# Optimization experiments

Measured on AMD Instinct MI355X. Metric: run time of the kernel, lower is better.

Reference implementation:

```python
import jax, jax.numpy as jnp
from jax import lax
import numpy as np

N, C, D, KNN = 32768, 1000, 1024, 16
EPS_EUC = 1e-12
EPS_COS = 1e-8
COS_THRESH = 0.85


def setup_inputs() -> dict:
    key = jax.random.key(0)
    k1, k2, k3 = jax.random.split(key, 3)
    feature = jax.random.normal(k1, (N, D), dtype=jnp.float32)
    pred = jax.random.normal(k2, (N, C), dtype=jnp.float32)
    unlabeled_index = jnp.arange(N, dtype=jnp.int64) if jax.config.jax_enable_x64 else jnp.arange(N, dtype=jnp.int32)
    # module state: centroids (from FeaturePool), top-N score buffer (init -1), fake index buffer (init -1)
    centroids = jax.random.normal(k3, (C, D), dtype=jnp.float32)
    pred_top_N = jnp.full((C, KNN), -1.0, dtype=jnp.float32)
    fake_index = jnp.full((C, KNN), -1, dtype=jnp.int32)
    return {"feature": feature, "pred": pred, "unlabeled_index": unlabeled_index,
            "centroids": centroids, "pred_top_N": pred_top_N, "fake_index": fake_index}


def reference(feature, pred, unlabeled_index, centroids, pred_top_N, fake_index):
    xx = jnp.sum(feature * feature, axis=1, keepdims=True)          # [N,1]
    yy = jnp.sum(centroids * centroids, axis=1)[None, :]            # [1,C]
    euc = jnp.sqrt(jnp.clip(xx + yy - 2.0 * (feature @ centroids.T), EPS_EUC, None))
    euc_id = jnp.argmin(euc, axis=1)                                # [N]

    scores = jnp.max(jax.nn.softmax(pred, axis=1), axis=1)          # [N] max softmax prob

    # cosine similarity of every sample to every centroid [N, C]
    f_n = feature / jnp.clip(jnp.linalg.norm(feature, axis=1, keepdims=True), EPS_COS, None)
    c_n = centroids / jnp.clip(jnp.linalg.norm(centroids, axis=1, keepdims=True), EPS_COS, None)
    cos = f_n @ c_n.T
    label_idx = jnp.argmax(cos, axis=1)                             # [N]
    cos_max = jnp.max(cos, axis=1)                                  # [N]

    # label[i] = label_idx if (cos-argmax == euc-argmin and cos_max > 0.85) else -1
    label = jnp.where((label_idx == euc_id) & (cos_max > COS_THRESH),
                      label_idx.astype(jnp.float32), -1.0)

    # sequential bounded top-N scatter update of (pred_top_N, fake_index)
    def step(carry, x):
        ptn, fidx = carry
        li, sc, ui = x
        row = ptn[li]                        # [KNN]
        mi = jnp.argmin(row)
        upd = sc > row[mi]
        ptn = ptn.at[li, mi].set(jnp.where(upd, sc, row[mi]))
        fidx = fidx.at[li, mi].set(jnp.where(upd, ui.astype(fidx.dtype), fidx[li, mi]))
        return (ptn, fidx), None

    (ptn_new, fidx_new), _ = lax.scan(step, (pred_top_N, fake_index),
                                      (label_idx, scores, unlabeled_index))
    return label, ptn_new, fidx_new
```

## Files before the change

kernel.cpp:

```cpp
#include <hip/hip_runtime.h>
#include <hip/hip_bf16.h>
#include <math.h>

#define NS 32768
#define NC 1000
#define CP 1024
#define DD 1024
#define KN 16

typedef __attribute__((ext_vector_type(8))) short bf16x8;
typedef __attribute__((ext_vector_type(4))) float f32x4;
typedef __attribute__((ext_vector_type(4))) float float4v;
typedef __attribute__((ext_vector_type(4))) int int4v;
typedef __attribute__((ext_vector_type(8))) unsigned short u16x8;
typedef __attribute__((ext_vector_type(4))) unsigned short u16x4;

__device__ __forceinline__ unsigned short f2bf(float f) {
  unsigned u = __float_as_uint(f);
  u += 0x7FFFu + ((u >> 16) & 1u);
  return (unsigned short)(u >> 16);
}
__device__ __forceinline__ float bf2f(unsigned short h) {
  return __uint_as_float(((unsigned)h) << 16);
}

#define GLL16(g, l) __builtin_amdgcn_global_load_lds( \
    (const __attribute__((address_space(1))) void*)(g), \
    (__attribute__((address_space(3))) void*)(l), 16, 0, 0)

__global__ __launch_bounds__(256) void k_cast_cent(
    const float* __restrict__ Cm, unsigned short* __restrict__ Cb,
    float* __restrict__ cnorm2, float* __restrict__ invc) {
  int c = blockIdx.x;
  int tid = threadIdx.x;
  float sq = 0.f;
  if (c < NC) {
    float4v v = ((const float4v*)(Cm + (size_t)c * DD))[tid];
    sq = v[0]*v[0] + v[1]*v[1] + v[2]*v[2] + v[3]*v[3];
    u16x4 o = { f2bf(v[0]), f2bf(v[1]), f2bf(v[2]), f2bf(v[3]) };
    *(u16x4*)(Cb + (size_t)c * DD + tid * 4) = o;
  } else {
    u16x4 z = { 0, 0, 0, 0 };
    *(u16x4*)(Cb + (size_t)c * DD + tid * 4) = z;
  }
  for (int off = 32; off; off >>= 1) sq += __shfl_xor(sq, off);
  __shared__ float red[4];
  int lane = tid & 63, wid = tid >> 6;
  if (!lane) red[wid] = sq;
  __syncthreads();
  if (!tid) {
    float s = red[0] + red[1] + red[2] + red[3];
    cnorm2[c] = s;
    float n = sqrtf(s); if (n < 1e-8f) n = 1e-8f;
    invc[c] = (c < NC) ? 1.0f / n : 0.0f;
  }
}

__global__ __launch_bounds__(256) void k_cast_feat(
    const float* __restrict__ A, unsigned short* __restrict__ Ab) {
  int t = blockIdx.x * 256 + threadIdx.x;
  const float4v* src = (const float4v*)A + (size_t)t * 2;
  float4v a = src[0], b = src[1];
  u16x8 o = { f2bf(a[0]), f2bf(a[1]), f2bf(a[2]), f2bf(a[3]),
              f2bf(b[0]), f2bf(b[1]), f2bf(b[2]), f2bf(b[3]) };
  *(u16x8*)(Ab + (size_t)t * 8) = o;
}

#define MF(a_, b_, c_) __builtin_amdgcn_mfma_f32_16x16x32_bf16(a_, b_, c_, 0, 0, 0)
#define RD(base_, i_) (*(const bf16x8*)((base_) + (i_) * 1024 + aoff))
#define SA(s_, b_) do { \
    GLL16(pA0 + (s_) * 32, ldsB + (b_) * 16384 + dA0); \
    GLL16(pA1 + (s_) * 32, ldsB + (b_) * 16384 + dA1); } while (0)
#define SB(s_, b_) do { \
    GLL16(pB0 + (s_) * 32, ldsB + 65536 + (b_) * 16384 + dA0); \
    GLL16(pB1 + (s_) * 32, ldsB + 65536 + (b_) * 16384 + dA1); } while (0)
#define VM4 asm volatile("s_waitcnt vmcnt(4)" ::: "memory")
#define VM0 asm volatile("s_waitcnt vmcnt(0)" ::: "memory")
#define MFMAC(A0_, A1_, A2_, A3_, M0) do { \
    acc[M0+0][0] = MF(A0_, bv0, acc[M0+0][0]); \
    acc[M0+0][1] = MF(A0_, bv1, acc[M0+0][1]); \
    acc[M0+0][2] = MF(A0_, bv2, acc[M0+0][2]); \
    acc[M0+0][3] = MF(A0_, bv3, acc[M0+0][3]); \
    acc[M0+1][0] = MF(A1_, bv0, acc[M0+1][0]); \
    acc[M0+1][1] = MF(A1_, bv1, acc[M0+1][1]); \
    acc[M0+1][2] = MF(A1_, bv2, acc[M0+1][2]); \
    acc[M0+1][3] = MF(A1_, bv3, acc[M0+1][3]); \
    acc[M0+2][0] = MF(A2_, bv0, acc[M0+2][0]); \
    acc[M0+2][1] = MF(A2_, bv1, acc[M0+2][1]); \
    acc[M0+2][2] = MF(A2_, bv2, acc[M0+2][2]); \
    acc[M0+2][3] = MF(A2_, bv3, acc[M0+2][3]); \
    acc[M0+3][0] = MF(A3_, bv0, acc[M0+3][0]); \
    acc[M0+3][1] = MF(A3_, bv1, acc[M0+3][1]); \
    acc[M0+3][2] = MF(A3_, bv2, acc[M0+3][2]); \
    acc[M0+3][3] = MF(A3_, bv3, acc[M0+3][3]); } while (0)
#define KSTEP(s_, STAGE_, GATE_) do { \
    const char* Ab_ = ldsB + ((s_) & 3) * 16384 + wrOff; \
    const char* Bb_ = ldsB + 65536 + ((s_) & 3) * 16384 + wcOff; \
    af0 = RD(Ab_, 0); af1 = RD(Ab_, 1); af2 = RD(Ab_, 2); af3 = RD(Ab_, 3); \
    bv0 = RD(Bb_, 0); bv1 = RD(Bb_, 1); bv2 = RD(Bb_, 2); bv3 = RD(Bb_, 3); \
    af4 = RD(Ab_, 4); af5 = RD(Ab_, 5); af6 = RD(Ab_, 6); af7 = RD(Ab_, 7); \
    STAGE_; \
    __builtin_amdgcn_s_setprio(1); \
    MFMAC(af0, af1, af2, af3, 0); \
    MFMAC(af4, af5, af6, af7, 4); \
    __builtin_amdgcn_s_setprio(0); \
    GATE_; \
    __builtin_amdgcn_s_barrier(); \
  } while (0)

__global__ __launch_bounds__(512, 1) void k_gemm(
    const unsigned short* __restrict__ A,
    const unsigned short* __restrict__ B,
    unsigned short* __restrict__ Dout) {
  __shared__ unsigned short lds[65536];
  char* ldsB = (char*)lds;
  int tid = threadIdx.x, lane = tid & 63, wid = tid >> 6;
  int wr = wid >> 2, wc = wid & 3;
  int bid = (blockIdx.x & 7) * 64 + (blockIdx.x >> 3);
  int cb = bid & 3, rb = bid >> 2;
  int brow = rb * 256, bcol = cb * 256;

  f32x4 acc[8][4];
#pragma unroll
  for (int m = 0; m < 8; ++m)
#pragma unroll
    for (int n = 0; n < 4; ++n) acc[m][n] = (f32x4){0.f, 0.f, 0.f, 0.f};

  int f0 = wid * 64 + lane, f1 = f0 + 512;
  int gl0 = (f0 & 3) ^ ((f0 >> 3) & 3);
  int gl1 = (f1 & 3) ^ ((f1 >> 3) & 3);
  const unsigned short* pA0 = A + (size_t)(brow + (f0 >> 2)) * DD + gl0 * 8;
  const unsigned short* pA1 = A + (size_t)(brow + (f1 >> 2)) * DD + gl1 * 8;
  const unsigned short* pB0 = B + (size_t)(bcol + (f0 >> 2)) * DD + gl0 * 8;
  const unsigned short* pB1 = B + (size_t)(bcol + (f1 >> 2)) * DD + gl1 * 8;
  int dA0 = f0 * 16, dA1 = f1 * 16;

  int aoff = (lane & 15) * 64 + (((lane >> 4) ^ ((lane >> 1) & 3)) * 16);
  int wrOff = wr * 8192;
  int wcOff = wc * 4096;

  bf16x8 af0, af1, af2, af3, af4, af5, af6, af7, bv0, bv1, bv2, bv3;

  SA(0, 0); SB(0, 0);
  SA(1, 1); SB(1, 1);
  VM4;
  __builtin_amdgcn_s_barrier();

  for (int s = 0; s < 30; ++s) {
    int bn = (s + 2) & 3;
    KSTEP(s, { SA(s + 2, bn); SB(s + 2, bn); }, VM4);
  }
  KSTEP(30, (void)0, VM0);
  KSTEP(31, (void)0, (void)0);

  int colb = bcol + wc * 64 + (lane & 15);
  int rowb = brow + wr * 128 + ((lane >> 4) << 2);
#pragma unroll
  for (int m = 0; m < 8; ++m)
#pragma unroll
    for (int n = 0; n < 4; ++n)
#pragma unroll
      for (int j = 0; j < 4; ++j)
        Dout[(size_t)(rowb + m * 16 + j) * CP + colb + n * 16] = f2bf(acc[m][n][j]);
}

__global__ __launch_bounds__(256) void k_score(
    const float* __restrict__ P, float* __restrict__ scores) {
  int i = blockIdx.x, tid = threadIdx.x;
  const float* row = P + (size_t)i * NC;
  bool act = tid < 250;
  float p0 = 0, p1 = 0, p2 = 0, p3 = 0, mx = -1e30f;
  if (act) {
    int b = tid * 4;
    p0 = row[b]; p1 = row[b + 1]; p2 = row[b + 2]; p3 = row[b + 3];
    mx = fmaxf(fmaxf(p0, p1), fmaxf(p2, p3));
  }
  for (int off = 32; off; off >>= 1) mx = fmaxf(mx, __shfl_xor(mx, off));
  __shared__ float wmax[4];
  __shared__ double wsum[4];
  int lane = tid & 63, wid = tid >> 6;
  if (!lane) wmax[wid] = mx;
  __syncthreads();
  float m = fmaxf(fmaxf(wmax[0], wmax[1]), fmaxf(wmax[2], wmax[3]));
  double s = 0.0;
  if (act)
    s = (double)__expf(p0 - m) + (double)__expf(p1 - m) +
        (double)__expf(p2 - m) + (double)__expf(p3 - m);
  for (int off = 32; off; off >>= 1) s += __shfl_xor(s, off);
  if (!lane) wsum[wid] = s;
  __syncthreads();
  if (!tid) scores[i] = (float)(1.0 / (wsum[0] + wsum[1] + wsum[2] + wsum[3]));
}

__global__ __launch_bounds__(256) void k_argmax(
    const unsigned short* __restrict__ Dot, const float* __restrict__ invc,
    const float* __restrict__ cnorm2, const float* __restrict__ feat,
    const float* __restrict__ cent, float* __restrict__ label_out,
    int* __restrict__ lidx) {
  __shared__ float s_inv[CP], s_cn[CP];
  int tid = threadIdx.x;
#pragma unroll
  for (int q = 0; q < 4; ++q) {
    int c = q * 256 + tid;
    s_inv[c] = invc[c]; s_cn[c] = cnorm2[c];
  }
  __syncthreads();
  int lane = tid & 63, wid = tid >> 6;
  int i = blockIdx.x * 4 + wid;
  const unsigned short* drow = Dot + (size_t)i * CP;

  float v[16];
  float dmax = -1e30f; int darg = CP;
  float emin = 1e30f;  int earg = CP;
#pragma unroll
  for (int it = 0; it < 16; ++it) {
    int c = it * 64 + lane;
    float val, ev;
    if (c < NC) {
      float d = bf2f(drow[c]);
      val = d * s_inv[c];
      ev = s_cn[c] - 2.0f * d;
    } else { val = -1e30f; ev = 1e30f; }
    v[it] = val;
    if (val > dmax) { dmax = val; darg = c; }
    if (ev < emin)  { emin = ev;  earg = c; }
  }
  for (int off = 32; off; off >>= 1) {
    float om = __shfl_xor(dmax, off); int oi = __shfl_xor(darg, off);
    if (om > dmax || (om == dmax && oi < darg)) { dmax = om; darg = oi; }
    float oe = __shfl_xor(emin, off); int oj = __shfl_xor(earg, off);
    if (oe < emin || (oe == emin && oj < earg)) { emin = oe; earg = oj; }
  }
  const float MARGIN = 0.15f;
  unsigned long long cmask[16]; int ccnt = 0;
#pragma unroll
  for (int it = 0; it < 16; ++it) {
    int c = it * 64 + lane;
    bool cand = (c < NC) && (v[it] >= dmax - MARGIN);
    cmask[it] = __ballot(cand);
    ccnt += __popcll(cmask[it]);
  }
  int finalArg = darg;
  double cosmax_d = -2.0;
  bool need = (ccnt > 1) || (dmax > 10.0f);
  if (need) {
    float xv[16]; double sx = 0.0;
    const float* xr = feat + (size_t)i * DD;
#pragma unroll
    for (int t = 0; t < 16; ++t) {
      float x = xr[t * 64 + lane]; xv[t] = x; sx += (double)x * (double)x;
    }
    for (int off = 32; off; off >>= 1) sx += __shfl_xor(sx, off);
    double nx = sqrt(sx); if (nx < 1e-8) nx = 1e-8;
    double best = -2.0; int besti = CP;
    for (int it = 0; it < 16; ++it) {
      unsigned long long mk = cmask[it];
      while (mk) {
        int b = __builtin_ctzll(mk); mk &= mk - 1;
        int c = it * 64 + b;
        const float* cr = cent + (size_t)c * DD;
        double s = 0.0, s2 = 0.0;
#pragma unroll
        for (int t = 0; t < 16; ++t) {
          double cv = (double)cr[t * 64 + lane];
          s += (double)xv[t] * cv; s2 += cv * cv;
        }
        for (int off = 32; off; off >>= 1) {
          s += __shfl_xor(s, off); s2 += __shfl_xor(s2, off);
        }
        double nc = sqrt(s2); if (nc < 1e-8) nc = 1e-8;
        double cs = s / (nx * nc);
        if (cs > best) { best = cs; besti = c; }
      }
    }
    finalArg = besti; cosmax_d = best;
  }
  if (!lane) {
    lidx[i] = finalArg;
    float lab = -1.0f;
    if (need && finalArg == earg && cosmax_d > 0.85) lab = (float)finalArg;
    label_out[i] = lab;
  }
}

__global__ __launch_bounds__(64) void k_scan(
    const int* __restrict__ lidx, const float* __restrict__ scores,
    const int* __restrict__ uidx, const float* __restrict__ ptn_in,
    const int* __restrict__ fidx_in, float* __restrict__ out_ptn,
    float* __restrict__ out_fidx) {
  int c = blockIdx.x;
  int lane = threadIdx.x;
  float row[KN]; int idx[KN];
#pragma unroll
  for (int j = 0; j < KN; ++j) {
    row[j] = ptn_in[c * KN + j];
    idx[j] = fidx_in[c * KN + j];
  }
  for (int base = 0; base < NS; base += 256) {
    int l0 = lidx[base + lane];
    int l1 = lidx[base + 64 + lane];
    int l2 = lidx[base + 128 + lane];
    int l3 = lidx[base + 192 + lane];
#pragma unroll
    for (int q = 0; q < 4; ++q) {
      int lab = (q == 0) ? l0 : (q == 1) ? l1 : (q == 2) ? l2 : l3;
      unsigned long long m = __ballot(lab == c);
      while (m) {
        int b = __builtin_ctzll(m); m &= m - 1;
        int i = base + q * 64 + b;
        float s = scores[i];
        int ui = uidx[i];
        int mi = 0; float mn = row[0];
#pragma unroll
        for (int t = 1; t < KN; ++t)
          if (row[t] < mn) { mn = row[t]; mi = t; }
        if (s > mn) {
#pragma unroll
          for (int t = 0; t < KN; ++t)
            if (t == mi) { row[t] = s; idx[t] = ui; }
        }
      }
    }
  }
  if (!lane) {
#pragma unroll
    for (int j = 0; j < KN; ++j) {
      out_ptn[c * KN + j] = row[j];
      out_fidx[c * KN + j] = (float)idx[j];
    }
  }
}

extern "C" void kernel_launch(void* const* d_in, const int* in_sizes, int n_in,
                              void* d_out, int out_size, void* d_ws, size_t ws_size,
                              hipStream_t stream) {
  const float* feature = (const float*)d_in[0];
  const float* pred    = (const float*)d_in[1];
  const int*   uidx    = (const int*)d_in[2];
  const float* cent    = (const float*)d_in[3];
  const float* ptn_in  = (const float*)d_in[4];
  const int*   fidx_in = (const int*)d_in[5];
  float* out = (float*)d_out;

  char* ws = (char*)d_ws;
  unsigned short* cent_bf = (unsigned short*)(ws);
  unsigned short* feat_bf = (unsigned short*)(ws + (2ull << 20));
  unsigned short* dot_bf  = (unsigned short*)(ws + (66ull << 20));
  float* scores = (float*)(ws + (130ull << 20));
  int*   lidx   = (int*)  (ws + (130ull << 20) + (128ull << 10));
  float* cnorm2 = (float*)(ws + (130ull << 20) + (256ull << 10));
  float* invc   = (float*)(ws + (130ull << 20) + (260ull << 10));

  hipLaunchKernelGGL(k_cast_cent, dim3(CP), dim3(256), 0, stream,
                     cent, cent_bf, cnorm2, invc);
  hipLaunchKernelGGL(k_cast_feat, dim3((NS * DD / 8) / 256), dim3(256), 0, stream,
                     feature, feat_bf);
  hipLaunchKernelGGL(k_gemm, dim3((NS / 256) * (CP / 256)), dim3(512), 0, stream,
                     feat_bf, cent_bf, dot_bf);
  hipLaunchKernelGGL(k_score, dim3(NS), dim3(256), 0, stream, pred, scores);
  hipLaunchKernelGGL(k_argmax, dim3(NS / 4), dim3(256), 0, stream,
                     dot_bf, invc, cnorm2, feature, cent, out, lidx);
  hipLaunchKernelGGL(k_scan, dim3(NC), dim3(64), 0, stream,
                     lidx, scores, uidx, ptn_in, fidx_in,
                     out + NS, out + NS + NC * KN);
}
```

Measured before the change: 235.1 us.

## Restructure GEMM main loop into 64-wide K tiles with four-phase pipelining

Reorganizes the bf16 MFMA GEMM main loop so that each iteration loads a 64-element K tile, double-buffered across two 64KB LDS halves. Each tile is processed in four phases, each with a half-M sub-block of MFMAs, and global-to-LDS loads for the next tile are interleaved between the phases. The change aims to smooth LDS reads and global prefetch against MFMA issue and to cut register pressure from holding twelve fragments at once. In exchange it adds an extra barrier per phase, four per tile, which could raise synchronisation overhead.

Result: slower. 240.1 us (+2.1%).

```diff
diff --git a/kernel.cpp b/kernel.cpp
--- a/kernel.cpp
+++ b/kernel.cpp
@@ -67,42 +67,44 @@
 }
 
 #define MF(a_, b_, c_) __builtin_amdgcn_mfma_f32_16x16x32_bf16(a_, b_, c_, 0, 0, 0)
-#define RD(base_, i_) (*(const bf16x8*)((base_) + (i_) * 1024 + aoff))
-#define SA(s_, b_) do { \
-    GLL16(pA0 + (s_) * 32, ldsB + (b_) * 16384 + dA0); \
-    GLL16(pA1 + (s_) * 32, ldsB + (b_) * 16384 + dA1); } while (0)
-#define SB(s_, b_) do { \
-    GLL16(pB0 + (s_) * 32, ldsB + 65536 + (b_) * 16384 + dA0); \
-    GLL16(pB1 + (s_) * 32, ldsB + 65536 + (b_) * 16384 + dA1); } while (0)
 #define VM4 asm volatile("s_waitcnt vmcnt(4)" ::: "memory")
 #define VM0 asm volatile("s_waitcnt vmcnt(0)" ::: "memory")
-#define MFMAC(A0_, A1_, A2_, A3_, M0) do { \
-    acc[M0+0][0] = MF(A0_, bv0, acc[M0+0][0]); \
-    acc[M0+0][1] = MF(A0_, bv1, acc[M0+0][1]); \
-    acc[M0+0][2] = MF(A0_, bv2, acc[M0+0][2]); \
-    acc[M0+0][3] = MF(A0_, bv3, acc[M0+0][3]); \
-    acc[M0+1][0] = MF(A1_, bv0, acc[M0+1][0]); \
-    acc[M0+1][1] = MF(A1_, bv1, acc[M0+1][1]); \
-    acc[M0+1][2] = MF(A1_, bv2, acc[M0+1][2]); \
-    acc[M0+1][3] = MF(A1_, bv3, acc[M0+1][3]); \
-    acc[M0+2][0] = MF(A2_, bv0, acc[M0+2][0]); \
-    acc[M0+2][1] = MF(A2_, bv1, acc[M0+2][1]); \
-    acc[M0+2][2] = MF(A2_, bv2, acc[M0+2][2]); \
-    acc[M0+2][3] = MF(A2_, bv3, acc[M0+2][3]); \
-    acc[M0+3][0] = MF(A3_, bv0, acc[M0+3][0]); \
-    acc[M0+3][1] = MF(A3_, bv1, acc[M0+3][1]); \
-    acc[M0+3][2] = MF(A3_, bv2, acc[M0+3][2]); \
-    acc[M0+3][3] = MF(A3_, bv3, acc[M0+3][3]); } while (0)
-#define KSTEP(s_, STAGE_, GATE_) do { \
-    const char* Ab_ = ldsB + ((s_) & 3) * 16384 + wrOff; \
-    const char* Bb_ = ldsB + 65536 + ((s_) & 3) * 16384 + wcOff; \
-    af0 = RD(Ab_, 0); af1 = RD(Ab_, 1); af2 = RD(Ab_, 2); af3 = RD(Ab_, 3); \
-    bv0 = RD(Bb_, 0); bv1 = RD(Bb_, 1); bv2 = RD(Bb_, 2); bv3 = RD(Bb_, 3); \
-    af4 = RD(Ab_, 4); af5 = RD(Ab_, 5); af6 = RD(Ab_, 6); af7 = RD(Ab_, 7); \
+#define SAK(t_, kh_) do { \
+    GLL16(gA0 + (t_) * 64 + (kh_) * 32, ldsB + (((t_) & 1) << 16) + ((kh_) * 2 + 0) * 8192 + dst); \
+    GLL16(gA1 + (t_) * 64 + (kh_) * 32, ldsB + (((t_) & 1) << 16) + ((kh_) * 2 + 1) * 8192 + dst); } while (0)
+#define SBK(t_, kh_) do { \
+    GLL16(gB0 + (t_) * 64 + (kh_) * 32, ldsB + (((t_) & 1) << 16) + 32768 + ((kh_) * 2 + 0) * 8192 + dst); \
+    GLL16(gB1 + (t_) * 64 + (kh_) * 32, ldsB + (((t_) & 1) << 16) + 32768 + ((kh_) * 2 + 1) * 8192 + dst); } while (0)
+#define PHASE(t_, kh_, mh_, STAGE_, GATE_) do { \
+    const char* Ab_ = ldsB + (((t_) & 1) << 16) + ((kh_) * 2 + wr) * 8192 + (mh_) * 4096 + aoff; \
+    const char* Bb_ = ldsB + (((t_) & 1) << 16) + 32768 + ((kh_) * 2 + (wc >> 1)) * 8192 + (wc & 1) * 4096 + aoff; \
+    bf16x8 a0 = *(const bf16x8*)(Ab_); \
+    bf16x8 a1 = *(const bf16x8*)(Ab_ + 1024); \
+    bf16x8 a2 = *(const bf16x8*)(Ab_ + 2048); \
+    bf16x8 a3 = *(const bf16x8*)(Ab_ + 3072); \
+    bf16x8 b0 = *(const bf16x8*)(Bb_); \
+    bf16x8 b1 = *(const bf16x8*)(Bb_ + 1024); \
+    bf16x8 b2 = *(const bf16x8*)(Bb_ + 2048); \
+    bf16x8 b3 = *(const bf16x8*)(Bb_ + 3072); \
     STAGE_; \
+    __builtin_amdgcn_s_barrier(); \
     __builtin_amdgcn_s_setprio(1); \
-    MFMAC(af0, af1, af2, af3, 0); \
-    MFMAC(af4, af5, af6, af7, 4); \
+    acc[(mh_)*4+0][0] = MF(a0, b0, acc[(mh_)*4+0][0]); \
+    acc[(mh_)*4+0][1] = MF(a0, b1, acc[(mh_)*4+0][1]); \
+    acc[(mh_)*4+0][2] = MF(a0, b2, acc[(mh_)*4+0][2]); \
+    acc[(mh_)*4+0][3] = MF(a0, b3, acc[(mh_)*4+0][3]); \
+    acc[(mh_)*4+1][0] = MF(a1, b0, acc[(mh_)*4+1][0]); \
+    acc[(mh_)*4+1][1] = MF(a1, b1, acc[(mh_)*4+1][1]); \
+    acc[(mh_)*4+1][2] = MF(a1, b2, acc[(mh_)*4+1][2]); \
+    acc[(mh_)*4+1][3] = MF(a1, b3, acc[(mh_)*4+1][3]); \
+    acc[(mh_)*4+2][0] = MF(a2, b0, acc[(mh_)*4+2][0]); \
+    acc[(mh_)*4+2][1] = MF(a2, b1, acc[(mh_)*4+2][1]); \
+    acc[(mh_)*4+2][2] = MF(a2, b2, acc[(mh_)*4+2][2]); \
+    acc[(mh_)*4+2][3] = MF(a2, b3, acc[(mh_)*4+2][3]); \
+    acc[(mh_)*4+3][0] = MF(a3, b0, acc[(mh_)*4+3][0]); \
+    acc[(mh_)*4+3][1] = MF(a3, b1, acc[(mh_)*4+3][1]); \
+    acc[(mh_)*4+3][2] = MF(a3, b2, acc[(mh_)*4+3][2]); \
+    acc[(mh_)*4+3][3] = MF(a3, b3, acc[(mh_)*4+3][3]); \
     __builtin_amdgcn_s_setprio(0); \
     GATE_; \
     __builtin_amdgcn_s_barrier(); \
@@ -126,32 +128,32 @@
 #pragma unroll
     for (int n = 0; n < 4; ++n) acc[m][n] = (f32x4){0.f, 0.f, 0.f, 0.f};
 
-  int f0 = wid * 64 + lane, f1 = f0 + 512;
-  int gl0 = (f0 & 3) ^ ((f0 >> 3) & 3);
-  int gl1 = (f1 & 3) ^ ((f1 >> 3) & 3);
-  const unsigned short* pA0 = A + (size_t)(brow + (f0 >> 2)) * DD + gl0 * 8;
-  const unsigned short* pA1 = A + (size_t)(brow + (f1 >> 2)) * DD + gl1 * 8;
-  const unsigned short* pB0 = B + (size_t)(bcol + (f0 >> 2)) * DD + gl0 * 8;
-  const unsigned short* pB1 = B + (size_t)(bcol + (f1 >> 2)) * DD + gl1 * 8;
-  int dA0 = f0 * 16, dA1 = f1 * 16;
+  int f = tid;
+  int gl = (f & 3) ^ ((f >> 3) & 3);
+  const unsigned short* gA0 = A + (size_t)(brow + (f >> 2)) * DD + gl * 8;
+  const unsigned short* gA1 = gA0 + (size_t)128 * DD;
+  const unsigned short* gB0 = B + (size_t)(bcol + (f >> 2)) * DD + gl * 8;
+  const unsigned short* gB1 = gB0 + (size_t)128 * DD;
+  int dst = f * 16;
 
   int aoff = (lane & 15) * 64 + (((lane >> 4) ^ ((lane >> 1) & 3)) * 16);
-  int wrOff = wr * 8192;
-  int wcOff = wc * 4096;
-
-  bf16x8 af0, af1, af2, af3, af4, af5, af6, af7, bv0, bv1, bv2, bv3;
-
-  SA(0, 0); SB(0, 0);
-  SA(1, 1); SB(1, 1);
+
+  SAK(0, 0); SBK(0, 0);
+  SAK(0, 1); SBK(0, 1);
   VM4;
   __builtin_amdgcn_s_barrier();
 
-  for (int s = 0; s < 30; ++s) {
-    int bn = (s + 2) & 3;
-    KSTEP(s, { SA(s + 2, bn); SB(s + 2, bn); }, VM4);
-  }
-  KSTEP(30, (void)0, VM0);
-  KSTEP(31, (void)0, (void)0);
+#pragma unroll 1
+  for (int t = 0; t < 15; ++t) {
+    PHASE(t, 0, 0, SAK(t + 1, 0), (void)0);
+    PHASE(t, 0, 1, SBK(t + 1, 0), VM4);
+    PHASE(t, 1, 0, SAK(t + 1, 1), (void)0);
+    PHASE(t, 1, 1, SBK(t + 1, 1), VM4);
+  }
+  PHASE(15, 0, 0, (void)0, (void)0);
+  PHASE(15, 0, 1, (void)0, VM0);
+  PHASE(15, 1, 0, (void)0, (void)0);
+  PHASE(15, 1, 1, (void)0, (void)0);
 
   int colb = bcol + wc * 64 + (lane & 15);
   int rowb = brow + wr * 128 + ((lane >> 4) << 2);
```
